# Optimization experiments

Hardware: AMD Instinct MI355X
Metric: run time of the kernel (lower is better)

Reference implementation:

```python
import jax, jax.numpy as jnp
import numpy as np

K_NBR = 64          # max_num_neighbors in radius()
RATIO1, R1 = 0.5, 0.2
RATIO2, R2 = 0.25, 0.4


def _mlp(h, params):
    # PyG MLP: Linear+ReLU per hidden layer, plain last layer (BN is identity at
    # init / eval with fresh running stats, so omitted).
    for w, b in params[:-1]:
        h = jax.nn.relu(h @ w + b)
    w, b = params[-1]
    return h @ w + b


def _fps(pos, S):
    # Farthest point sampling, deterministic start at index 0. pos: [N,3]
    min_d = jnp.sum((pos - pos[0]) ** 2, axis=-1)

    def body(md, _):
        i = jnp.argmax(md)
        md = jnp.minimum(md, jnp.sum((pos - pos[i]) ** 2, axis=-1))
        return md, i

    _, idxs = jax.lax.scan(body, min_d, None, length=S - 1)
    return jnp.concatenate([jnp.zeros((1,), idxs.dtype), idxs])  # [S]


def _sa(x, pos, S, r, params):
    # One SAModule for a single cloud. x: [N,C], pos: [N,3]
    sel = _fps(pos, S)
    pos_s = pos[sel]                                                   # [S,3]
    d2 = jnp.sum((pos_s[:, None, :] - pos[None, :, :]) ** 2, axis=-1)  # [S,N]
    score = jnp.where(d2 <= r * r, -d2, -jnp.inf)
    vals, nbr = jax.lax.top_k(score, K_NBR)      # <=64 nearest within radius r
    mask = vals > -jnp.inf                       # [S,K]; center always valid
    # PointNetConv message: cat([x_j, pos_j - pos_i]) -> local MLP -> max-aggr
    feats = jnp.concatenate([x[nbr], pos[nbr] - pos_s[:, None, :]], axis=-1)
    h = _mlp(feats, params)                      # [S,K,Cout]
    h = jnp.max(jnp.where(mask[..., None], h, -jnp.inf), axis=1)
    return h, pos_s


def _forward(data, p1, p2, p3, fc_w, fc_b):
    B, N, _ = data.shape
    S1 = int(np.ceil(N * RATIO1))
    S2 = int(np.ceil(S1 * RATIO2))
    # sa1 is called with x = pos = raw coordinates
    x1, pos1 = jax.vmap(lambda p: _sa(p, p, S1, R1, p1))(data)
    x2, pos2 = jax.vmap(lambda x, p: _sa(x, p, S2, R2, p2))(x1, pos1)
    # GlobalSAModule: MLP on cat([x, pos]) then global max pool per cloud
    g = jnp.max(_mlp(jnp.concatenate([x2, pos2], axis=-1), p3), axis=1)  # [B,1024]
    return g @ fc_w + fc_b


def setup_inputs() -> dict:
    key = jax.random.key(0)
    ks = jax.random.split(key, 16)
    B, N = 4, 4096
    inp = {"data": jax.random.uniform(ks[0], (B, N, 3), jnp.float32)}
    dims = {"sa1": [6, 64, 64, 128],
            "sa2": [131, 128, 128, 256],
            "sa3": [259, 256, 512, 1024]}
    i = 1
    for name, ds in dims.items():
        for l in range(len(ds) - 1):
            fi, fo = ds[l], ds[l + 1]
            inp[f"{name}_w{l + 1}"] = (jax.random.normal(ks[i], (fi, fo), jnp.float32)
                                       / np.float32(np.sqrt(fi)))
            inp[f"{name}_b{l + 1}"] = jnp.zeros((fo,), jnp.float32)
            i += 1
    inp["fc_w"] = jax.random.normal(ks[i], (1024, 256), jnp.float32) / np.float32(32.0)
    inp["fc_b"] = jnp.zeros((256,), jnp.float32)
    return inp


def reference(data, sa1_w1, sa1_b1, sa1_w2, sa1_b2, sa1_w3, sa1_b3,
              sa2_w1, sa2_b1, sa2_w2, sa2_b2, sa2_w3, sa2_b3,
              sa3_w1, sa3_b1, sa3_w2, sa3_b2, sa3_w3, sa3_b3,
              fc_w, fc_b):
    p1 = [(sa1_w1, sa1_b1), (sa1_w2, sa1_b2), (sa1_w3, sa1_b3)]
    p2 = [(sa2_w1, sa2_b1), (sa2_w2, sa2_b2), (sa2_w3, sa2_b3)]
    p3 = [(sa3_w1, sa3_b1), (sa3_w2, sa3_b2), (sa3_w3, sa3_b3)]
    return _forward(data, p1, p2, p3, fc_w, fc_b)  # [B, 256]
```

## Files before the change

kernel.cpp:

```cpp
#include <hip/hip_runtime.h>


#define DEVFN __device__ __forceinline__

DEVFN float d2_exact(float ax, float ay, float az, float bx, float by, float bz) {
    float dx = __fsub_rn(ax, bx);
    float dy = __fsub_rn(ay, by);
    float dz = __fsub_rn(az, bz);
    return __fadd_rn(__fadd_rn(__fmul_rn(dx, dx), __fmul_rn(dy, dy)), __fmul_rn(dz, dz));
}

DEVFN unsigned long long u64max(unsigned long long a, unsigned long long b) {
    return a > b ? a : b;
}

template <int R>
DEVFN unsigned long long dpp_ror16_u64(unsigned long long x) {
    int lo = (int)(unsigned)(x & 0xFFFFFFFFull);
    int hi = (int)(unsigned)(x >> 32);
    lo = __builtin_amdgcn_update_dpp(lo, lo, 0x120 | R, 0xF, 0xF, false);
    hi = __builtin_amdgcn_update_dpp(hi, hi, 0x120 | R, 0xF, 0xF, false);
    return ((unsigned long long)(unsigned)hi << 32) | (unsigned)lo;
}

DEVFN unsigned long long rl_u64(unsigned long long x, int lane) {
    unsigned l = (unsigned)__builtin_amdgcn_readlane((int)(unsigned)(x & 0xFFFFFFFFull), lane);
    unsigned h = (unsigned)__builtin_amdgcn_readlane((int)(unsigned)(x >> 32), lane);
    return ((unsigned long long)h << 32) | l;
}

template <int N, int S, int NT>
DEVFN void run_fps(const float* sx, const float* sy, const float* sz,
                   unsigned long long* sPack,
                   int* selLds) {
    constexpr int PPT = N / NT;
    constexpr int NW = NT / 64;
    const int tid = threadIdx.x;
    float px[PPT], py[PPT], pz[PPT], md[PPT];
    unsigned loc[PPT];
#pragma unroll
    for (int i = 0; i < PPT; ++i) {
        int idx = tid * PPT + i;
        px[i] = sx[idx]; py[i] = sy[idx]; pz[i] = sz[idx];
        md[i] = __builtin_inff();
        loc[i] = 0xFFFFFFFFu - (unsigned)idx;
    }
    if (tid == 0) selLds[0] = 0;
    int cur = 0;
    for (int s = 1; s < S; ++s) {
        float ax = sx[cur], ay = sy[cur], az = sz[cur];
        unsigned long long tq[PPT];
#pragma unroll
        for (int i = 0; i < PPT; ++i) {
            float d = d2_exact(px[i], py[i], pz[i], ax, ay, az);
            float m = fminf(md[i], d);
            md[i] = m;
            tq[i] = ((unsigned long long)__float_as_uint(m) << 32) |
                    (unsigned long long)loc[i];
        }
#pragma unroll
        for (int w = PPT / 2; w >= 1; w >>= 1)
#pragma unroll
            for (int i = 0; i < w; ++i) tq[i] = u64max(tq[i], tq[i + w]);

        unsigned long long pk = tq[0];
        pk = u64max(pk, dpp_ror16_u64<8>(pk));
        pk = u64max(pk, dpp_ror16_u64<4>(pk));
        pk = u64max(pk, dpp_ror16_u64<2>(pk));
        pk = u64max(pk, dpp_ror16_u64<1>(pk));

        unsigned long long wmax = u64max(u64max(rl_u64(pk, 0), rl_u64(pk, 16)),
                                         u64max(rl_u64(pk, 32), rl_u64(pk, 48)));

        unsigned long long* sp = sPack + (s & 1) * NW;
        if ((tid & 63) == 0) sp[tid >> 6] = wmax;
        __syncthreads();

        unsigned long long win;
        if constexpr (NW == 8) {
            const ulonglong2* sp2 = (const ulonglong2*)sp;
            ulonglong2 q0 = sp2[0], q1 = sp2[1], q2 = sp2[2], q3 = sp2[3];
            unsigned long long m01 = u64max(u64max(q0.x, q0.y), u64max(q1.x, q1.y));
            unsigned long long m23 = u64max(u64max(q2.x, q2.y), u64max(q3.x, q3.y));
            win = u64max(m01, m23);
        } else {
            const ulonglong2* sp2 = (const ulonglong2*)sp;
            ulonglong2 q0 = sp2[0], q1 = sp2[1];
            win = u64max(u64max(q0.x, q0.y), u64max(q1.x, q1.y));
        }

        cur = (int)(0xFFFFFFFFu - (unsigned)(win & 0xFFFFFFFFull));
        if (tid == 0) selLds[s] = cur;
    }
}

template <int N, int CAP>
DEVFN void nbr_body(const float* __restrict__ pos,
                    const float cx, const float cy, const float cz,
                    const float rsq, const int c,
                    int* __restrict__ nbr, int* __restrict__ cnt,
                    float* sDw, int* sIw) {
    const int lane = threadIdx.x & 63;
    int count = 0;
    for (int j = lane; j < N; j += 64) {
        float d = d2_exact(cx, cy, cz, pos[j * 3 + 0], pos[j * 3 + 1], pos[j * 3 + 2]);
        bool pred = (d <= rsq);
        unsigned long long m = __ballot(pred);
        int wpos = count + __popcll(m & ((1ull << lane) - 1ull));
        if (pred && wpos < CAP) { sDw[wpos] = d; sIw[wpos] = j; }
        count += __popcll(m);
    }
    if (count > CAP) count = CAP;

    for (int t = lane; t < count; t += 64) {
        float d = sDw[t]; int id = sIw[t];
        int rank = 0;
        int j0 = 0;
        for (; j0 + 4 <= count; j0 += 4) {
            float4 dj = *(const float4*)&sDw[j0];
            int4   ij = *(const int4*)&sIw[j0];
            rank += (dj.x < d || (dj.x == d && ij.x < id)) ? 1 : 0;
            rank += (dj.y < d || (dj.y == d && ij.y < id)) ? 1 : 0;
            rank += (dj.z < d || (dj.z == d && ij.z < id)) ? 1 : 0;
            rank += (dj.w < d || (dj.w == d && ij.w < id)) ? 1 : 0;
        }
        for (; j0 < count; ++j0) {
            float dj = sDw[j0]; int ij = sIw[j0];
            rank += (dj < d || (dj == d && ij < id)) ? 1 : 0;
        }
        if (rank < 64) nbr[(size_t)c * 64 + rank] = id;
    }
    if (lane == 0) cnt[c] = count < 64 ? count : 64;
}

__global__ __launch_bounds__(512) void fpsnbr_kernel(
    const float* __restrict__ data,
    float* __restrict__ mdG,
    int* __restrict__ selG,
    float* __restrict__ pos1,
    const int sb, const int se,
    const float rsq, int* __restrict__ nbr1, int* __restrict__ cnt1,
    const int s0)
{
    __shared__ __align__(16) char raw[65536];
    const int tid = threadIdx.x;

    if (blockIdx.x >= 4) {
        float* sD = (float*)raw;
        int*   sI = (int*)(raw + 32768);
        const int wid = tid >> 6;
        const int g = (int)(blockIdx.x - 4) * 8 + wid;
        const int b = g >> 9;
        const int s = s0 + (g & 511);
        const int c = b * 2048 + s;
        const float cx = pos1[(size_t)c * 3 + 0];
        const float cy = pos1[(size_t)c * 3 + 1];
        const float cz = pos1[(size_t)c * 3 + 2];
        nbr_body<4096, 1024>(data + (size_t)b * 4096 * 3, cx, cy, cz, rsq, c,
                             nbr1, cnt1, sD + wid * 1024, sI + wid * 1024);
        return;
    }

    constexpr int N = 4096, NT = 512, PPT = N / NT, NW = NT / 64;
    float* sx = (float*)raw;
    float* sy = sx + 4096;
    float* sz = sy + 4096;
    unsigned long long* sPack = (unsigned long long*)(raw + 49152);
    int* sSel = (int*)(raw + 49280);

    const int b = blockIdx.x;
    const float* p = data + (size_t)b * N * 3;
    for (int i = tid; i < N; i += NT) {
        sx[i] = p[i * 3 + 0]; sy[i] = p[i * 3 + 1]; sz[i] = p[i * 3 + 2];
    }
    __syncthreads();

    float px[PPT], py[PPT], pz[PPT], md[PPT];
    const bool first = (sb == 1);
#pragma unroll
    for (int i = 0; i < PPT; ++i) {
        int idx = tid * PPT + i;
        px[i] = sx[idx]; py[i] = sy[idx]; pz[i] = sz[idx];
        md[i] = first ? __builtin_inff() : mdG[(size_t)b * N + idx];
    }
    int cur = first ? 0 : selG[(size_t)b * 2048 + sb - 1];
    if (first && tid == 0) selG[(size_t)b * 2048] = 0;
    const unsigned lob = 0xFFFFFFFFu - (unsigned)(tid * PPT);

    for (int s = sb; s < se; ++s) {
        float ax = sx[cur], ay = sy[cur], az = sz[cur];
        float mm[PPT];
#pragma unroll
        for (int i = 0; i < PPT; ++i) {
            float d = d2_exact(px[i], py[i], pz[i], ax, ay, az);
            float m = fminf(md[i], d);
            md[i] = m; mm[i] = m;
        }
        float a0 = fmaxf(mm[0], mm[4]), a1 = fmaxf(mm[1], mm[5]);
        float a2 = fmaxf(mm[2], mm[6]), a3 = fmaxf(mm[3], mm[7]);
        float b0 = fmaxf(a0, a2), b1 = fmaxf(a1, a3);
        float mloc = fmaxf(b0, b1);
        int li = 7;
#pragma unroll
        for (int i = 6; i >= 0; --i) li = (mm[i] == mloc) ? i : li;

        unsigned long long k0 =
            ((unsigned long long)__float_as_uint(mloc) << 32) |
            (unsigned long long)(lob - (unsigned)li);

        k0 = u64max(k0, dpp_ror16_u64<8>(k0));
        k0 = u64max(k0, dpp_ror16_u64<4>(k0));
        k0 = u64max(k0, dpp_ror16_u64<2>(k0));
        k0 = u64max(k0, dpp_ror16_u64<1>(k0));

        unsigned long long wmax = u64max(u64max(rl_u64(k0, 0), rl_u64(k0, 16)),
                                         u64max(rl_u64(k0, 32), rl_u64(k0, 48)));

        unsigned long long* sp = sPack + (s & 1) * NW;
        if ((tid & 63) == 0) sp[tid >> 6] = wmax;
        __syncthreads();

        const ulonglong2* sp2 = (const ulonglong2*)sp;
        ulonglong2 q0 = sp2[0], q1 = sp2[1], q2 = sp2[2], q3 = sp2[3];
        unsigned long long m01 = u64max(u64max(q0.x, q0.y), u64max(q1.x, q1.y));
        unsigned long long m23 = u64max(u64max(q2.x, q2.y), u64max(q3.x, q3.y));
        unsigned long long win = u64max(m01, m23);

        cur = (int)(0xFFFFFFFFu - (unsigned)(win & 0xFFFFFFFFull));
        if (tid == 0) sSel[s - sb] = cur;
    }
    __syncthreads();

    if (se < 2048) {
#pragma unroll
        for (int i = 0; i < PPT; ++i)
            mdG[(size_t)b * N + tid * PPT + i] = md[i];
    }
    if (tid == 0) selG[(size_t)b * 2048 + se - 1] = cur;

    float* p1 = pos1 + (size_t)b * 2048 * 3;
    const int sb0 = first ? 0 : sb;
    for (int s = sb0 + tid; s < se; s += NT) {
        int idx = (s == 0) ? 0 : sSel[s - sb];
        p1[s * 3 + 0] = sx[idx]; p1[s * 3 + 1] = sy[idx]; p1[s * 3 + 2] = sz[idx];
    }
}

__global__ __launch_bounds__(512) void fps2nbr_kernel(
    const float* __restrict__ data,
    const float* __restrict__ pos1,
    float* __restrict__ pos2,
    const float rsq, int* __restrict__ nbr1, int* __restrict__ cnt1,
    const int s0)
{
    __shared__ __align__(16) char raw[65536];
    const int tid = threadIdx.x;

    if (blockIdx.x >= 4) {
        float* sD = (float*)raw;
        int*   sI = (int*)(raw + 32768);
        const int wid = tid >> 6;
        const int g = (int)(blockIdx.x - 4) * 8 + wid;
        const int b = g >> 9;
        const int s = s0 + (g & 511);
        const int c = b * 2048 + s;
        const float cx = pos1[(size_t)c * 3 + 0];
        const float cy = pos1[(size_t)c * 3 + 1];
        const float cz = pos1[(size_t)c * 3 + 2];
        nbr_body<4096, 1024>(data + (size_t)b * 4096 * 3, cx, cy, cz, rsq, c,
                             nbr1, cnt1, sD + wid * 1024, sI + wid * 1024);
        return;
    }

    float* sx = (float*)raw;
    float* sy = sx + 2048;
    float* sz = sy + 2048;
    int* sSel2 = (int*)(raw + 24576);
    unsigned long long* sPack2 = (unsigned long long*)(raw + 26624);

    const int b = blockIdx.x;
    const float* p1 = pos1 + (size_t)b * 2048 * 3;
    for (int i = tid; i < 2048; i += 512) {
        sx[i] = p1[i * 3 + 0]; sy[i] = p1[i * 3 + 1]; sz[i] = p1[i * 3 + 2];
    }
    __syncthreads();

    run_fps<2048, 512, 512>(sx, sy, sz, sPack2, sSel2);
    __syncthreads();

    float* p2 = pos2 + (size_t)b * 512 * 3;
    {
        int si = sSel2[tid];
        p2[tid * 3 + 0] = sx[si]; p2[tid * 3 + 1] = sy[si]; p2[tid * 3 + 2] = sz[si];
    }
}

DEVFN void tile44_fma(const float* __restrict__ aBase, int aStride,
                      const float* __restrict__ wBase, int wStride,
                      int nk4, float (&acc)[4][4]) {
    for (int k4 = 0; k4 < nk4; ++k4) {
        float a[4][4], w[4][4];
#pragma unroll
        for (int i = 0; i < 4; ++i) {
            float4 t = *(const float4*)(aBase + i * aStride + k4 * 4);
            a[i][0] = t.x; a[i][1] = t.y; a[i][2] = t.z; a[i][3] = t.w;
        }
#pragma unroll
        for (int kk = 0; kk < 4; ++kk) {
            float4 t = *(const float4*)(wBase + (size_t)(k4 * 4 + kk) * wStride);
            w[kk][0] = t.x; w[kk][1] = t.y; w[kk][2] = t.z; w[kk][3] = t.w;
        }
#pragma unroll
        for (int kk = 0; kk < 4; ++kk)
#pragma unroll
            for (int i = 0; i < 4; ++i)
#pragma unroll
                for (int j = 0; j < 4; ++j)
                    acc[i][j] = fmaf(a[i][kk], w[kk][j], acc[i][j]);
    }
}

DEVFN void tile48_fma(const float* __restrict__ aBase, int aStride,
                      const float* __restrict__ wBase, int wStride,
                      int nk4, float (&acc)[4][8]) {
    for (int k4 = 0; k4 < nk4; ++k4) {
        float a[4][4];
#pragma unroll
        for (int i = 0; i < 4; ++i) {
            float4 t = *(const float4*)(aBase + i * aStride + k4 * 4);
            a[i][0] = t.x; a[i][1] = t.y; a[i][2] = t.z; a[i][3] = t.w;
        }
#pragma unroll
        for (int kk = 0; kk < 4; ++kk) {
            float4 t0 = *(const float4*)(wBase + (size_t)(k4 * 4 + kk) * wStride);
            float4 t1 = *(const float4*)(wBase + (size_t)(k4 * 4 + kk) * wStride + 4);
            float w_[8] = {t0.x, t0.y, t0.z, t0.w, t1.x, t1.y, t1.z, t1.w};
#pragma unroll
            for (int i = 0; i < 4; ++i)
#pragma unroll
                for (int j = 0; j < 8; ++j)
                    acc[i][j] = fmaf(a[i][kk], w_[j], acc[i][j]);
        }
    }
}

__global__ __launch_bounds__(256) void mlp1nbr2_kernel(
    const float* __restrict__ pos,
    const float* __restrict__ ctr,
    const int* __restrict__ nbr, const int* __restrict__ cnt,
    const float* __restrict__ w1, const float* __restrict__ b1,
    const float* __restrict__ w2, const float* __restrict__ b2,
    const float* __restrict__ w3, const float* __restrict__ b3,
    float* __restrict__ x1,
    const float* __restrict__ pos1,
    const float* __restrict__ pos2,
    const float rsq2, int* __restrict__ nbr2, int* __restrict__ cnt2)
{
    __shared__ __align__(16) float smem[15424];
    const int tid = threadIdx.x;

    if (blockIdx.x < 512) {
        float* sD = smem;
        int*   sI = (int*)(smem + 6144);
        const int wid = tid >> 6;
        const int c = (int)blockIdx.x * 4 + wid;
        const int b = c >> 9;
        const float cx = pos2[(size_t)c * 3 + 0];
        const float cy = pos2[(size_t)c * 3 + 1];
        const float cz = pos2[(size_t)c * 3 + 2];
        nbr_body<2048, 1536>(pos1 + (size_t)b * 2048 * 3, cx, cy, cz, rsq2, c,
                             nbr2, cnt2, sD + wid * 1536, sI + wid * 1536);
        return;
    }

    float* sFeat = smem;
    float* sW    = smem + 576;
    float* sH1   = smem + 4672;
    float* sH2   = smem + 9024;
    float* sRed  = smem + 13376;

    const int c = blockIdx.x - 512;
    const int b = c >> 11;
    const int valid = cnt[c];

    if (tid < 64) {
        const int r = tid;
        float fx = 0.f, fy = 0.f, fz = 0.f, dx = 0.f, dy = 0.f, dz = 0.f;
        if (r < valid) {
            int j = nbr[(size_t)c * 64 + r];
            const float* pj = pos + ((size_t)b * 4096 + j) * 3;
            fx = pj[0]; fy = pj[1]; fz = pj[2];
            dx = fx - ctr[c * 3 + 0]; dy = fy - ctr[c * 3 + 1]; dz = fz - ctr[c * 3 + 2];
        }
        float* fr = sFeat + r * 9;
        fr[0] = fx; fr[1] = fy; fr[2] = fz; fr[3] = dx; fr[4] = dy; fr[5] = dz;
    }
    for (int l = tid; l < 4096; l += 256) sW[l] = w2[l];
    __syncthreads();

    {
        const int r = tid & 63, c0 = (tid >> 6) * 16;
        float acc[16];
#pragma unroll
        for (int q = 0; q < 16; ++q) acc[q] = b1[c0 + q];
#pragma unroll
        for (int k = 0; k < 6; ++k) {
            float a = sFeat[r * 9 + k];
#pragma unroll
            for (int q = 0; q < 16; ++q) acc[q] = fmaf(a, w1[k * 64 + c0 + q], acc[q]);
        }
        float* hr = sH1 + r * 68 + c0;
#pragma unroll
        for (int q = 0; q < 16; ++q) hr[q] = fmaxf(acc[q], 0.f);
    }
    __syncthreads();

    {
        const int r0 = (tid >> 4) * 4, c0 = (tid & 15) * 4;
        float acc[4][4];
#pragma unroll
        for (int i = 0; i < 4; ++i)
#pragma unroll
            for (int j = 0; j < 4; ++j) acc[i][j] = b2[c0 + j];
        tile44_fma(sH1 + r0 * 68, 68, sW + c0, 64, 16, acc);
#pragma unroll
        for (int i = 0; i < 4; ++i)
#pragma unroll
            for (int j = 0; j < 4; ++j)
                sH2[(r0 + i) * 68 + c0 + j] = fmaxf(acc[i][j], 0.f);
    }
    __syncthreads();

    for (int l = tid; l < 8192; l += 256) sW[l] = w3[l];
    __syncthreads();
    {
        const int r0 = (tid >> 4) * 4, c0 = (tid & 15) * 8;
        float acc[4][8];
#pragma unroll
        for (int i = 0; i < 4; ++i)
#pragma unroll
            for (int j = 0; j < 8; ++j) acc[i][j] = 0.f;
        tile48_fma(sH2 + r0 * 68, 68, sW + c0, 128, 16, acc);
        float pm[8];
#pragma unroll
        for (int j = 0; j < 8; ++j) pm[j] = -__builtin_inff();
#pragma unroll
        for (int i = 0; i < 4; ++i)
            if (r0 + i < valid)
#pragma unroll
                for (int j = 0; j < 8; ++j) pm[j] = fmaxf(pm[j], acc[i][j]);
#pragma unroll
        for (int j = 0; j < 8; ++j) sRed[(tid >> 4) * 128 + c0 + j] = pm[j];
    }
    __syncthreads();
    if (tid < 128) {
        float m = -__builtin_inff();
#pragma unroll
        for (int g = 0; g < 16; ++g) m = fmaxf(m, sRed[g * 128 + tid]);
        x1[(size_t)c * 128 + tid] = m + b3[tid];
    }
}

__global__ __launch_bounds__(512, 4) void mlp2_kernel(
    const float* __restrict__ x1,
    const float* __restrict__ pos1,
    const float* __restrict__ ctr,
    const int* __restrict__ nbr, const int* __restrict__ cnt,
    const float* __restrict__ w1, const float* __restrict__ b1,
    const float* __restrict__ w2, const float* __restrict__ b2,
    const float* __restrict__ w3, const float* __restrict__ b3,
    float* __restrict__ x2)
{
    __shared__ __align__(16) float sF[64 * 132];
    __shared__ __align__(16) float sH[64 * 132];
    float* sRed = sH;

    const int tid = threadIdx.x;
    const int c = blockIdx.x;
    const int b = c >> 9;
    const int valid = cnt[c];
    const float cx = ctr[c * 3 + 0], cy = ctr[c * 3 + 1], cz = ctr[c * 3 + 2];

    {
        const int r = tid >> 3, t8 = tid & 7;
        float* fr = sF + r * 132;
        if (r < valid) {
            int j = nbr[(size_t)c * 64 + r];
            const float* xp = x1 + ((size_t)b * 2048 + j) * 128;
#pragma unroll
            for (int q = 0; q < 4; ++q) {
                float4 v = *(const float4*)(xp + t8 * 16 + q * 4);
                fr[t8 * 16 + q * 4 + 0] = v.x; fr[t8 * 16 + q * 4 + 1] = v.y;
                fr[t8 * 16 + q * 4 + 2] = v.z; fr[t8 * 16 + q * 4 + 3] = v.w;
            }
            if (t8 == 0) {
                const float* pj = pos1 + ((size_t)b * 2048 + j) * 3;
                fr[128] = pj[0] - cx; fr[129] = pj[1] - cy; fr[130] = pj[2] - cz;
                fr[131] = 0.f;
            }
        } else {
#pragma unroll
            for (int q = 0; q < 16; ++q) fr[t8 * 16 + q] = 0.f;
            if (t8 == 0) { fr[128] = 0.f; fr[129] = 0.f; fr[130] = 0.f; fr[131] = 0.f; }
        }
    }
    __syncthreads();

    const int r0 = (tid >> 5) * 4;
    const int c0 = (tid & 31) * 4;
    const int c8 = (tid & 31) * 8;

    {
        float acc[4][4];
#pragma unroll
        for (int i = 0; i < 4; ++i)
#pragma unroll
            for (int j = 0; j < 4; ++j) acc[i][j] = b1[c0 + j];
        tile44_fma(sF + r0 * 132, 132, w1 + c0, 128, 32, acc);
        for (int k = 128; k < 131; ++k) {
            float4 wv = *(const float4*)(w1 + (size_t)k * 128 + c0);
            float w_[4] = {wv.x, wv.y, wv.z, wv.w};
#pragma unroll
            for (int i = 0; i < 4; ++i) {
                float a = sF[(r0 + i) * 132 + k];
#pragma unroll
                for (int j = 0; j < 4; ++j) acc[i][j] = fmaf(a, w_[j], acc[i][j]);
            }
        }
#pragma unroll
        for (int i = 0; i < 4; ++i)
#pragma unroll
            for (int j = 0; j < 4; ++j)
                sH[(r0 + i) * 132 + c0 + j] = fmaxf(acc[i][j], 0.f);
    }
    __syncthreads();

    {
        float acc[4][4];
#pragma unroll
        for (int i = 0; i < 4; ++i)
#pragma unroll
            for (int j = 0; j < 4; ++j) acc[i][j] = b2[c0 + j];
        tile44_fma(sH + r0 * 132, 132, w2 + c0, 128, 32, acc);
#pragma unroll
        for (int i = 0; i < 4; ++i)
#pragma unroll
            for (int j = 0; j < 4; ++j)
                sF[(r0 + i) * 132 + c0 + j] = fmaxf(acc[i][j], 0.f);
    }
    __syncthreads();

    {
        float acc[4][8];
#pragma unroll
        for (int i = 0; i < 4; ++i)
#pragma unroll
            for (int j = 0; j < 8; ++j) acc[i][j] = 0.f;
        tile48_fma(sF + r0 * 132, 132, w3 + c8, 256, 32, acc);
        float pm[8];
#pragma unroll
        for (int j = 0; j < 8; ++j) pm[j] = -__builtin_inff();
#pragma unroll
        for (int i = 0; i < 4; ++i)
            if (r0 + i < valid)
#pragma unroll
                for (int j = 0; j < 8; ++j) pm[j] = fmaxf(pm[j], acc[i][j]);
#pragma unroll
        for (int j = 0; j < 8; ++j) sRed[(tid >> 5) * 256 + c8 + j] = pm[j];
    }
    __syncthreads();
    if (tid < 256) {
        float m = -__builtin_inff();
#pragma unroll
        for (int g = 0; g < 16; ++g) m = fmaxf(m, sRed[g * 256 + tid]);
        x2[(size_t)c * 256 + tid] = m + b3[tid];
    }
}

__global__ __launch_bounds__(256) void gemm1f_kernel(const float* __restrict__ x2,
                                                     const float* __restrict__ pos2,
                                                     const float* __restrict__ W,
                                                     const float* __restrict__ bias,
                                                     float* __restrict__ C) {
    constexpr int K = 259, Nc = 256;
    __shared__ __align__(16) float sA[64 * 36];
    __shared__ __align__(16) float sB[32 * 68];
    const int tid = threadIdx.x;
    const int row0 = blockIdx.y * 64, col0 = blockIdx.x * 64;
    const int r0 = (tid >> 4) * 4, c0 = (tid & 15) * 4;
    float acc[4][4];
#pragma unroll
    for (int i = 0; i < 4; ++i)
#pragma unroll
        for (int j = 0; j < 4; ++j) acc[i][j] = 0.f;

    for (int kb = 0; kb < K; kb += 32) {
        for (int l = tid; l < 64 * 32; l += 256) {
            int r = l >> 5, k = l & 31;
            int gk = kb + k;
            float av = 0.f;
            if (gk < K) {
                int row = row0 + r;
                av = (gk < 256) ? x2[(size_t)row * 256 + gk]
                                : pos2[row * 3 + (gk - 256)];
            }
            sA[r * 36 + k] = av;
        }
        for (int l = tid; l < 32 * 64; l += 256) {
            int k = l >> 6, cc = l & 63;
            sB[k * 68 + cc] = (kb + k < K) ? W[(size_t)(kb + k) * Nc + col0 + cc] : 0.f;
        }
        __syncthreads();
        tile44_fma(sA + r0 * 36, 36, sB + c0, 68, 8, acc);
        __syncthreads();
    }
#pragma unroll
    for (int i = 0; i < 4; ++i)
#pragma unroll
        for (int j = 0; j < 4; ++j)
            C[(size_t)(row0 + r0 + i) * Nc + col0 + c0 + j] =
                fmaxf(acc[i][j] + bias[col0 + c0 + j], 0.f);
}

__global__ __launch_bounds__(256) void gemm_kernel(const float* __restrict__ A,
                                                   const float* __restrict__ W,
                                                   const float* __restrict__ bias,
                                                   float* __restrict__ C,
                                                   int M, int K, int Nc, int relu) {
    __shared__ __align__(16) float sA[64 * 36];
    __shared__ __align__(16) float sB[32 * 68];
    const int tid = threadIdx.x;
    const int row0 = blockIdx.y * 64, col0 = blockIdx.x * 64;
    const int r0 = (tid >> 4) * 4, c0 = (tid & 15) * 4;
    float acc[4][4];
#pragma unroll
    for (int i = 0; i < 4; ++i)
#pragma unroll
        for (int j = 0; j < 4; ++j) acc[i][j] = 0.f;

    for (int kb = 0; kb < K; kb += 32) {
        for (int l = tid; l < 64 * 32; l += 256) {
            int r = l >> 5, k = l & 31;
            sA[r * 36 + k] = (kb + k < K) ? A[(size_t)(row0 + r) * K + kb + k] : 0.f;
        }
        for (int l = tid; l < 32 * 64; l += 256) {
            int k = l >> 6, cc = l & 63;
            sB[k * 68 + cc] = (kb + k < K) ? W[(size_t)(kb + k) * Nc + col0 + cc] : 0.f;
        }
        __syncthreads();
        tile44_fma(sA + r0 * 36, 36, sB + c0, 68, 8, acc);
        __syncthreads();
    }
#pragma unroll
    for (int i = 0; i < 4; ++i)
#pragma unroll
        for (int j = 0; j < 4; ++j) {
            float v = acc[i][j] + bias[col0 + c0 + j];
            if (relu) v = fmaxf(v, 0.f);
            C[(size_t)(row0 + r0 + i) * Nc + col0 + c0 + j] = v;
        }
}

__global__ __launch_bounds__(1024) void mpfc_kernel(const float* __restrict__ h,
                                                    const float* __restrict__ w,
                                                    const float* __restrict__ bias,
                                                    float* __restrict__ out) {
    __shared__ float sG[1024];
    __shared__ float sP[4][256];
    const int b = blockIdx.x, tid = threadIdx.x;

    float m = -__builtin_inff();
    const float* hp = h + (size_t)b * 512 * 1024 + tid;
    for (int r = 0; r < 512; ++r) m = fmaxf(m, hp[(size_t)r * 1024]);
    sG[tid] = m;
    __syncthreads();

    const int c = tid & 255, kc = tid >> 8;
    float acc = 0.f;
    const float* wp = w + (size_t)(kc * 256) * 256 + c;
    const float* gp = sG + kc * 256;
    for (int k = 0; k < 256; ++k) acc = fmaf(gp[k], wp[(size_t)k * 256], acc);
    sP[kc][c] = acc;
    __syncthreads();
    if (tid < 256)
        out[b * 256 + tid] = ((sP[0][tid] + sP[1][tid]) + (sP[2][tid] + sP[3][tid]))
                             + bias[tid];
}

extern "C" void kernel_launch(void* const* d_in, const int* in_sizes, int n_in,
                              void* d_out, int out_size, void* d_ws, size_t ws_size,
                              hipStream_t stream) {
    const float* data  = (const float*)d_in[0];
    const float* s1w1  = (const float*)d_in[1];
    const float* s1b1  = (const float*)d_in[2];
    const float* s1w2  = (const float*)d_in[3];
    const float* s1b2  = (const float*)d_in[4];
    const float* s1w3  = (const float*)d_in[5];
    const float* s1b3  = (const float*)d_in[6];
    const float* s2w1  = (const float*)d_in[7];
    const float* s2b1  = (const float*)d_in[8];
    const float* s2w2  = (const float*)d_in[9];
    const float* s2b2  = (const float*)d_in[10];
    const float* s2w3  = (const float*)d_in[11];
    const float* s2b3  = (const float*)d_in[12];
    const float* s3w1  = (const float*)d_in[13];
    const float* s3b1  = (const float*)d_in[14];
    const float* s3w2  = (const float*)d_in[15];
    const float* s3b2  = (const float*)d_in[16];
    const float* s3w3  = (const float*)d_in[17];
    const float* s3b3  = (const float*)d_in[18];
    const float* fcw   = (const float*)d_in[19];
    const float* fcb   = (const float*)d_in[20];
    float* out = (float*)d_out;

    char* ws = (char*)d_ws;
    size_t o = 0;
    auto nxt = [&](size_t bytes) {
        size_t r = o;
        o += (bytes + 255) & ~(size_t)255;
        return r;
    };
    float* pos1 = (float*)(ws + nxt(4 * 2048 * 3 * 4));
    float* pos2 = (float*)(ws + nxt(4 * 512 * 3 * 4));
    float* mdG  = (float*)(ws + nxt(4 * 4096 * 4));
    int*   selG = (int*)(ws + nxt(4 * 2048 * 4));
    int*   nbr1 = (int*)(ws + nxt((size_t)8192 * 64 * 4));
    int*   cnt1 = (int*)(ws + nxt(8192 * 4));
    int*   nbr2 = (int*)(ws + nxt((size_t)2048 * 64 * 4));
    int*   cnt2 = (int*)(ws + nxt(2048 * 4));
    float* x1   = (float*)(ws + nxt((size_t)8192 * 128 * 4));
    float* x2   = (float*)(ws + nxt((size_t)2048 * 256 * 4));
    float* h1   = (float*)(ws + nxt((size_t)2048 * 256 * 4));
    float* h2   = (float*)(ws + nxt((size_t)2048 * 512 * 4));
    float* h3   = (float*)(ws + nxt((size_t)2048 * 1024 * 4));

    const float R1SQ = (float)(0.2 * 0.2);
    const float R2SQ = (float)(0.4 * 0.4);

    fpsnbr_kernel<<<4, 512, 0, stream>>>(data, mdG, selG, pos1, 1, 512,
                                         R1SQ, nbr1, cnt1, 0);
    fpsnbr_kernel<<<260, 512, 0, stream>>>(data, mdG, selG, pos1, 512, 1024,
                                           R1SQ, nbr1, cnt1, 0);
    fpsnbr_kernel<<<260, 512, 0, stream>>>(data, mdG, selG, pos1, 1024, 1536,
                                           R1SQ, nbr1, cnt1, 512);
    fpsnbr_kernel<<<260, 512, 0, stream>>>(data, mdG, selG, pos1, 1536, 2048,
                                           R1SQ, nbr1, cnt1, 1024);
    fps2nbr_kernel<<<260, 512, 0, stream>>>(data, pos1, pos2,
                                            R1SQ, nbr1, cnt1, 1536);
    mlp1nbr2_kernel<<<512 + 8192, 256, 0, stream>>>(data, pos1, nbr1, cnt1,
                                                    s1w1, s1b1, s1w2, s1b2,
                                                    s1w3, s1b3, x1,
                                                    pos1, pos2, R2SQ, nbr2, cnt2);
    mlp2_kernel<<<2048, 512, 0, stream>>>(x1, pos1, pos2, nbr2, cnt2,
                                          s2w1, s2b1, s2w2, s2b2, s2w3, s2b3, x2);
    gemm1f_kernel<<<dim3(4, 32), 256, 0, stream>>>(x2, pos2, s3w1, s3b1, h1);
    gemm_kernel<<<dim3(8, 32), 256, 0, stream>>>(h1, s3w2, s3b2, h2, 2048, 256, 512, 1);
    gemm_kernel<<<dim3(16, 32), 256, 0, stream>>>(h2, s3w3, s3b3, h3, 2048, 512, 1024, 0);
    mpfc_kernel<<<4, 1024, 0, stream>>>(h3, fcw, fcb, out);
}
```

Baseline: 2.647 ms.

## Overlap SA1 MLP chunks with serial FPS and neighbor search stages

Splits the SA1 MLP into per-chunk work and runs it in the same launches as the remaining FPS chunks and neighbor searches, so the MLP for already-grouped centers overlaps the serial 4-block FPS loop. The MLP body is also retiled for 512 threads, reading w2 and w3 directly from global memory instead of staging w2 in LDS. The stages are pipelined so each chunk's MLP runs one stage after its neighbors are found. Risks are more LDS per block (64 KB), lower occupancy for the MLP work, and interference with the latency-critical FPS blocks.

Result: slower. 4.255 ms (+60.7%).

```diff
diff --git a/kernel.cpp b/kernel.cpp
--- a/kernel.cpp
+++ b/kernel.cpp
@@ -29,10 +29,97 @@
     return ((unsigned long long)h << 32) | l;
 }
 
+DEVFN void fps_chunk_body(const float* __restrict__ data, float* __restrict__ mdG,
+                          int* __restrict__ selG, float* __restrict__ pos1,
+                          const int sb, const int se, char* raw) {
+    constexpr int N = 4096, NT = 512, PPT = N / NT, NW = NT / 64;
+    float* sx = (float*)raw;
+    float* sy = sx + 4096;
+    float* sz = sy + 4096;
+    unsigned long long* sPack = (unsigned long long*)(raw + 49152);
+    int* sSel = (int*)(raw + 49280);
+
+    const int b = blockIdx.x, tid = threadIdx.x;
+    const float* p = data + (size_t)b * N * 3;
+    for (int i = tid; i < N; i += NT) {
+        sx[i] = p[i * 3 + 0]; sy[i] = p[i * 3 + 1]; sz[i] = p[i * 3 + 2];
+    }
+    __syncthreads();
+
+    float px[PPT], py[PPT], pz[PPT], md[PPT];
+    const bool first = (sb == 1);
+#pragma unroll
+    for (int i = 0; i < PPT; ++i) {
+        int idx = tid * PPT + i;
+        px[i] = sx[idx]; py[i] = sy[idx]; pz[i] = sz[idx];
+        md[i] = first ? __builtin_inff() : mdG[(size_t)b * N + idx];
+    }
+    int cur = first ? 0 : selG[(size_t)b * 2048 + sb - 1];
+    if (first && tid == 0) selG[(size_t)b * 2048] = 0;
+    const unsigned lob = 0xFFFFFFFFu - (unsigned)(tid * PPT);
+
+    for (int s = sb; s < se; ++s) {
+        float ax = sx[cur], ay = sy[cur], az = sz[cur];
+        float mm[PPT];
+#pragma unroll
+        for (int i = 0; i < PPT; ++i) {
+            float d = d2_exact(px[i], py[i], pz[i], ax, ay, az);
+            float m = fminf(md[i], d);
+            md[i] = m; mm[i] = m;
+        }
+        float a0 = fmaxf(mm[0], mm[4]), a1 = fmaxf(mm[1], mm[5]);
+        float a2 = fmaxf(mm[2], mm[6]), a3 = fmaxf(mm[3], mm[7]);
+        float b0 = fmaxf(a0, a2), b1 = fmaxf(a1, a3);
+        float mloc = fmaxf(b0, b1);
+        int li = 7;
+#pragma unroll
+        for (int i = 6; i >= 0; --i) li = (mm[i] == mloc) ? i : li;
+
+        unsigned long long k0 =
+            ((unsigned long long)__float_as_uint(mloc) << 32) |
+            (unsigned long long)(lob - (unsigned)li);
+
+        k0 = u64max(k0, dpp_ror16_u64<8>(k0));
+        k0 = u64max(k0, dpp_ror16_u64<4>(k0));
+        k0 = u64max(k0, dpp_ror16_u64<2>(k0));
+        k0 = u64max(k0, dpp_ror16_u64<1>(k0));
+
+        unsigned long long wmax = u64max(u64max(rl_u64(k0, 0), rl_u64(k0, 16)),
+                                         u64max(rl_u64(k0, 32), rl_u64(k0, 48)));
+
+        unsigned long long* sp = sPack + (s & 1) * NW;
+        if ((tid & 63) == 0) sp[tid >> 6] = wmax;
+        __syncthreads();
+
+        const ulonglong2* sp2 = (const ulonglong2*)sp;
+        ulonglong2 q0 = sp2[0], q1 = sp2[1], q2 = sp2[2], q3 = sp2[3];
+        unsigned long long m01 = u64max(u64max(q0.x, q0.y), u64max(q1.x, q1.y));
+        unsigned long long m23 = u64max(u64max(q2.x, q2.y), u64max(q3.x, q3.y));
+        unsigned long long win = u64max(m01, m23);
+
+        cur = (int)(0xFFFFFFFFu - (unsigned)(win & 0xFFFFFFFFull));
+        if (tid == 0) sSel[s - sb] = cur;
+    }
+    __syncthreads();
+
+    if (se < 2048) {
+#pragma unroll
+        for (int i = 0; i < PPT; ++i)
+            mdG[(size_t)b * N + tid * PPT + i] = md[i];
+    }
+    if (tid == 0) selG[(size_t)b * 2048 + se - 1] = cur;
+
+    float* p1 = pos1 + (size_t)b * 2048 * 3;
+    const int sb0 = (sb == 1) ? 0 : sb;
+    for (int s = sb0 + tid; s < se; s += NT) {
+        int idx = (s == 0) ? 0 : sSel[s - sb];
+        p1[s * 3 + 0] = sx[idx]; p1[s * 3 + 1] = sy[idx]; p1[s * 3 + 2] = sz[idx];
+    }
+}
+
 template <int N, int S, int NT>
 DEVFN void run_fps(const float* sx, const float* sy, const float* sz,
-                   unsigned long long* sPack,
-                   int* selLds) {
+                   unsigned long long* sPack, int* selLds) {
     constexpr int PPT = N / NT;
     constexpr int NW = NT / 64;
     const int tid = threadIdx.x;
@@ -133,254 +220,17 @@
     if (lane == 0) cnt[c] = count < 64 ? count : 64;
 }
 
-__global__ __launch_bounds__(512) void fpsnbr_kernel(
-    const float* __restrict__ data,
-    float* __restrict__ mdG,
-    int* __restrict__ selG,
-    float* __restrict__ pos1,
-    const int sb, const int se,
-    const float rsq, int* __restrict__ nbr1, int* __restrict__ cnt1,
-    const int s0)
-{
-    __shared__ __align__(16) char raw[65536];
+DEVFN void mlp1_body(const float* __restrict__ pos, const float* __restrict__ ctr,
+                     const int* __restrict__ nbr, const int* __restrict__ cnt,
+                     const float* __restrict__ w1, const float* __restrict__ b1,
+                     const float* __restrict__ w2, const float* __restrict__ b2,
+                     const float* __restrict__ w3, const float* __restrict__ b3,
+                     float* __restrict__ x1, const int c, const int b, float* smemf) {
+    float* sFeat = smemf;
+    float* sH1   = smemf + 576;
+    float* sH2   = smemf + 4928;
+    float* sRed  = smemf + 9280;
     const int tid = threadIdx.x;
-
-    if (blockIdx.x >= 4) {
-        float* sD = (float*)raw;
-        int*   sI = (int*)(raw + 32768);
-        const int wid = tid >> 6;
-        const int g = (int)(blockIdx.x - 4) * 8 + wid;
-        const int b = g >> 9;
-        const int s = s0 + (g & 511);
-        const int c = b * 2048 + s;
-        const float cx = pos1[(size_t)c * 3 + 0];
-        const float cy = pos1[(size_t)c * 3 + 1];
-        const float cz = pos1[(size_t)c * 3 + 2];
-        nbr_body<4096, 1024>(data + (size_t)b * 4096 * 3, cx, cy, cz, rsq, c,
-                             nbr1, cnt1, sD + wid * 1024, sI + wid * 1024);
-        return;
-    }
-
-    constexpr int N = 4096, NT = 512, PPT = N / NT, NW = NT / 64;
-    float* sx = (float*)raw;
-    float* sy = sx + 4096;
-    float* sz = sy + 4096;
-    unsigned long long* sPack = (unsigned long long*)(raw + 49152);
-    int* sSel = (int*)(raw + 49280);
-
-    const int b = blockIdx.x;
-    const float* p = data + (size_t)b * N * 3;
-    for (int i = tid; i < N; i += NT) {
-        sx[i] = p[i * 3 + 0]; sy[i] = p[i * 3 + 1]; sz[i] = p[i * 3 + 2];
-    }
-    __syncthreads();
-
-    float px[PPT], py[PPT], pz[PPT], md[PPT];
-    const bool first = (sb == 1);
-#pragma unroll
-    for (int i = 0; i < PPT; ++i) {
-        int idx = tid * PPT + i;
-        px[i] = sx[idx]; py[i] = sy[idx]; pz[i] = sz[idx];
-        md[i] = first ? __builtin_inff() : mdG[(size_t)b * N + idx];
-    }
-    int cur = first ? 0 : selG[(size_t)b * 2048 + sb - 1];
-    if (first && tid == 0) selG[(size_t)b * 2048] = 0;
-    const unsigned lob = 0xFFFFFFFFu - (unsigned)(tid * PPT);
-
-    for (int s = sb; s < se; ++s) {
-        float ax = sx[cur], ay = sy[cur], az = sz[cur];
-        float mm[PPT];
-#pragma unroll
-        for (int i = 0; i < PPT; ++i) {
-            float d = d2_exact(px[i], py[i], pz[i], ax, ay, az);
-            float m = fminf(md[i], d);
-            md[i] = m; mm[i] = m;
-        }
-        float a0 = fmaxf(mm[0], mm[4]), a1 = fmaxf(mm[1], mm[5]);
-        float a2 = fmaxf(mm[2], mm[6]), a3 = fmaxf(mm[3], mm[7]);
-        float b0 = fmaxf(a0, a2), b1 = fmaxf(a1, a3);
-        float mloc = fmaxf(b0, b1);
-        int li = 7;
-#pragma unroll
-        for (int i = 6; i >= 0; --i) li = (mm[i] == mloc) ? i : li;
-
-        unsigned long long k0 =
-            ((unsigned long long)__float_as_uint(mloc) << 32) |
-            (unsigned long long)(lob - (unsigned)li);
-
-        k0 = u64max(k0, dpp_ror16_u64<8>(k0));
-        k0 = u64max(k0, dpp_ror16_u64<4>(k0));
-        k0 = u64max(k0, dpp_ror16_u64<2>(k0));
-        k0 = u64max(k0, dpp_ror16_u64<1>(k0));
-
-        unsigned long long wmax = u64max(u64max(rl_u64(k0, 0), rl_u64(k0, 16)),
-                                         u64max(rl_u64(k0, 32), rl_u64(k0, 48)));
-
-        unsigned long long* sp = sPack + (s & 1) * NW;
-        if ((tid & 63) == 0) sp[tid >> 6] = wmax;
-        __syncthreads();
-
-        const ulonglong2* sp2 = (const ulonglong2*)sp;
-        ulonglong2 q0 = sp2[0], q1 = sp2[1], q2 = sp2[2], q3 = sp2[3];
-        unsigned long long m01 = u64max(u64max(q0.x, q0.y), u64max(q1.x, q1.y));
-        unsigned long long m23 = u64max(u64max(q2.x, q2.y), u64max(q3.x, q3.y));
-        unsigned long long win = u64max(m01, m23);
-
-        cur = (int)(0xFFFFFFFFu - (unsigned)(win & 0xFFFFFFFFull));
-        if (tid == 0) sSel[s - sb] = cur;
-    }
-    __syncthreads();
-
-    if (se < 2048) {
-#pragma unroll
-        for (int i = 0; i < PPT; ++i)
-            mdG[(size_t)b * N + tid * PPT + i] = md[i];
-    }
-    if (tid == 0) selG[(size_t)b * 2048 + se - 1] = cur;
-
-    float* p1 = pos1 + (size_t)b * 2048 * 3;
-    const int sb0 = first ? 0 : sb;
-    for (int s = sb0 + tid; s < se; s += NT) {
-        int idx = (s == 0) ? 0 : sSel[s - sb];
-        p1[s * 3 + 0] = sx[idx]; p1[s * 3 + 1] = sy[idx]; p1[s * 3 + 2] = sz[idx];
-    }
-}
-
-__global__ __launch_bounds__(512) void fps2nbr_kernel(
-    const float* __restrict__ data,
-    const float* __restrict__ pos1,
-    float* __restrict__ pos2,
-    const float rsq, int* __restrict__ nbr1, int* __restrict__ cnt1,
-    const int s0)
-{
-    __shared__ __align__(16) char raw[65536];
-    const int tid = threadIdx.x;
-
-    if (blockIdx.x >= 4) {
-        float* sD = (float*)raw;
-        int*   sI = (int*)(raw + 32768);
-        const int wid = tid >> 6;
-        const int g = (int)(blockIdx.x - 4) * 8 + wid;
-        const int b = g >> 9;
-        const int s = s0 + (g & 511);
-        const int c = b * 2048 + s;
-        const float cx = pos1[(size_t)c * 3 + 0];
-        const float cy = pos1[(size_t)c * 3 + 1];
-        const float cz = pos1[(size_t)c * 3 + 2];
-        nbr_body<4096, 1024>(data + (size_t)b * 4096 * 3, cx, cy, cz, rsq, c,
-                             nbr1, cnt1, sD + wid * 1024, sI + wid * 1024);
-        return;
-    }
-
-    float* sx = (float*)raw;
-    float* sy = sx + 2048;
-    float* sz = sy + 2048;
-    int* sSel2 = (int*)(raw + 24576);
-    unsigned long long* sPack2 = (unsigned long long*)(raw + 26624);
-
-    const int b = blockIdx.x;
-    const float* p1 = pos1 + (size_t)b * 2048 * 3;
-    for (int i = tid; i < 2048; i += 512) {
-        sx[i] = p1[i * 3 + 0]; sy[i] = p1[i * 3 + 1]; sz[i] = p1[i * 3 + 2];
-    }
-    __syncthreads();
-
-    run_fps<2048, 512, 512>(sx, sy, sz, sPack2, sSel2);
-    __syncthreads();
-
-    float* p2 = pos2 + (size_t)b * 512 * 3;
-    {
-        int si = sSel2[tid];
-        p2[tid * 3 + 0] = sx[si]; p2[tid * 3 + 1] = sy[si]; p2[tid * 3 + 2] = sz[si];
-    }
-}
-
-DEVFN void tile44_fma(const float* __restrict__ aBase, int aStride,
-                      const float* __restrict__ wBase, int wStride,
-                      int nk4, float (&acc)[4][4]) {
-    for (int k4 = 0; k4 < nk4; ++k4) {
-        float a[4][4], w[4][4];
-#pragma unroll
-        for (int i = 0; i < 4; ++i) {
-            float4 t = *(const float4*)(aBase + i * aStride + k4 * 4);
-            a[i][0] = t.x; a[i][1] = t.y; a[i][2] = t.z; a[i][3] = t.w;
-        }
-#pragma unroll
-        for (int kk = 0; kk < 4; ++kk) {
-            float4 t = *(const float4*)(wBase + (size_t)(k4 * 4 + kk) * wStride);
-            w[kk][0] = t.x; w[kk][1] = t.y; w[kk][2] = t.z; w[kk][3] = t.w;
-        }
-#pragma unroll
-        for (int kk = 0; kk < 4; ++kk)
-#pragma unroll
-            for (int i = 0; i < 4; ++i)
-#pragma unroll
-                for (int j = 0; j < 4; ++j)
-                    acc[i][j] = fmaf(a[i][kk], w[kk][j], acc[i][j]);
-    }
-}
-
-DEVFN void tile48_fma(const float* __restrict__ aBase, int aStride,
-                      const float* __restrict__ wBase, int wStride,
-                      int nk4, float (&acc)[4][8]) {
-    for (int k4 = 0; k4 < nk4; ++k4) {
-        float a[4][4];
-#pragma unroll
-        for (int i = 0; i < 4; ++i) {
-            float4 t = *(const float4*)(aBase + i * aStride + k4 * 4);
-            a[i][0] = t.x; a[i][1] = t.y; a[i][2] = t.z; a[i][3] = t.w;
-        }
-#pragma unroll
-        for (int kk = 0; kk < 4; ++kk) {
-            float4 t0 = *(const float4*)(wBase + (size_t)(k4 * 4 + kk) * wStride);
-            float4 t1 = *(const float4*)(wBase + (size_t)(k4 * 4 + kk) * wStride + 4);
-            float w_[8] = {t0.x, t0.y, t0.z, t0.w, t1.x, t1.y, t1.z, t1.w};
-#pragma unroll
-            for (int i = 0; i < 4; ++i)
-#pragma unroll
-                for (int j = 0; j < 8; ++j)
-                    acc[i][j] = fmaf(a[i][kk], w_[j], acc[i][j]);
-        }
-    }
-}
-
-__global__ __launch_bounds__(256) void mlp1nbr2_kernel(
-    const float* __restrict__ pos,
-    const float* __restrict__ ctr,
-    const int* __restrict__ nbr, const int* __restrict__ cnt,
-    const float* __restrict__ w1, const float* __restrict__ b1,
-    const float* __restrict__ w2, const float* __restrict__ b2,
-    const float* __restrict__ w3, const float* __restrict__ b3,
-    float* __restrict__ x1,
-    const float* __restrict__ pos1,
-    const float* __restrict__ pos2,
-    const float rsq2, int* __restrict__ nbr2, int* __restrict__ cnt2)
-{
-    __shared__ __align__(16) float smem[15424];
-    const int tid = threadIdx.x;
-
-    if (blockIdx.x < 512) {
-        float* sD = smem;
-        int*   sI = (int*)(smem + 6144);
-        const int wid = tid >> 6;
-        const int c = (int)blockIdx.x * 4 + wid;
-        const int b = c >> 9;
-        const float cx = pos2[(size_t)c * 3 + 0];
-        const float cy = pos2[(size_t)c * 3 + 1];
-        const float cz = pos2[(size_t)c * 3 + 2];
-        nbr_body<2048, 1536>(pos1 + (size_t)b * 2048 * 3, cx, cy, cz, rsq2, c,
-                             nbr2, cnt2, sD + wid * 1536, sI + wid * 1536);
-        return;
-    }
-
-    float* sFeat = smem;
-    float* sW    = smem + 576;
-    float* sH1   = smem + 4672;
-    float* sH2   = smem + 9024;
-    float* sRed  = smem + 13376;
-
-    const int c = blockIdx.x - 512;
-    const int b = c >> 11;
     const int valid = cnt[c];
 
     if (tid < 64) {
@@ -395,62 +245,89 @@
         float* fr = sFeat + r * 9;
         fr[0] = fx; fr[1] = fy; fr[2] = fz; fr[3] = dx; fr[4] = dy; fr[5] = dz;
     }
-    for (int l = tid; l < 4096; l += 256) sW[l] = w2[l];
     __syncthreads();
 
     {
-        const int r = tid & 63, c0 = (tid >> 6) * 16;
-        float acc[16];
-#pragma unroll
-        for (int q = 0; q < 16; ++q) acc[q] = b1[c0 + q];
+        const int r = tid & 63, c0 = (tid >> 6) * 8;
+        float acc[8];
+#pragma unroll
+        for (int q = 0; q < 8; ++q) acc[q] = b1[c0 + q];
 #pragma unroll
         for (int k = 0; k < 6; ++k) {
             float a = sFeat[r * 9 + k];
 #pragma unroll
-            for (int q = 0; q < 16; ++q) acc[q] = fmaf(a, w1[k * 64 + c0 + q], acc[q]);
+            for (int q = 0; q < 8; ++q) acc[q] = fmaf(a, w1[k * 64 + c0 + q], acc[q]);
         }
         float* hr = sH1 + r * 68 + c0;
 #pragma unroll
-        for (int q = 0; q < 16; ++q) hr[q] = fmaxf(acc[q], 0.f);
+        for (int q = 0; q < 8; ++q) hr[q] = fmaxf(acc[q], 0.f);
     }
     __syncthreads();
 
     {
-        const int r0 = (tid >> 4) * 4, c0 = (tid & 15) * 4;
+        const int rg = tid >> 4, c0 = (tid & 15) * 4;
+        float acc0[4], acc1[4];
+#pragma unroll
+        for (int j = 0; j < 4; ++j) { acc0[j] = b2[c0 + j]; acc1[j] = b2[c0 + j]; }
+        for (int k4 = 0; k4 < 16; ++k4) {
+            float4 t0 = *(const float4*)(sH1 + rg * 68 + k4 * 4);
+            float4 t1 = *(const float4*)(sH1 + (rg + 32) * 68 + k4 * 4);
+            float a0_[4] = {t0.x, t0.y, t0.z, t0.w};
+            float a1_[4] = {t1.x, t1.y, t1.z, t1.w};
+#pragma unroll
+            for (int kk = 0; kk < 4; ++kk) {
+                float4 wv = *(const float4*)(w2 + (size_t)(k4 * 4 + kk) * 64 + c0);
+                float w_[4] = {wv.x, wv.y, wv.z, wv.w};
+#pragma unroll
+                for (int j = 0; j < 4; ++j) {
+                    acc0[j] = fmaf(a0_[kk], w_[j], acc0[j]);
+                    acc1[j] = fmaf(a1_[kk], w_[j], acc1[j]);
+                }
+            }
+        }
+#pragma unroll
+        for (int j = 0; j < 4; ++j) {
+            sH2[rg * 68 + c0 + j]        = fmaxf(acc0[j], 0.f);
+            sH2[(rg + 32) * 68 + c0 + j] = fmaxf(acc1[j], 0.f);
+        }
+    }
+    __syncthreads();
+
+    {
+        const int rg = tid >> 5, c0 = (tid & 31) * 4;
         float acc[4][4];
 #pragma unroll
         for (int i = 0; i < 4; ++i)
 #pragma unroll
-            for (int j = 0; j < 4; ++j) acc[i][j] = b2[c0 + j];
-        tile44_fma(sH1 + r0 * 68, 68, sW + c0, 64, 16, acc);
+            for (int j = 0; j < 4; ++j) acc[i][j] = 0.f;
+        for (int k4 = 0; k4 < 16; ++k4) {
+            float a[4][4];
+#pragma unroll
+            for (int i = 0; i < 4; ++i) {
+                float4 t = *(const float4*)(sH2 + (rg + 16 * i) * 68 + k4 * 4);
+                a[i][0] = t.x; a[i][1] = t.y; a[i][2] = t.z; a[i][3] = t.w;
+            }
+#pragma unroll
+            for (int kk = 0; kk < 4; ++kk) {
+                float4 wv = *(const float4*)(w3 + (size_t)(k4 * 4 + kk) * 128 + c0);
+                float w_[4] = {wv.x, wv.y, wv.z, wv.w};
+#pragma unroll
+                for (int i = 0; i < 4; ++i)
+#pragma unroll
+                    for (int j = 0; j < 4; ++j)
+                        acc[i][j] = fmaf(a[i][kk], w_[j], acc[i][j]);
+            }
+        }
+        float pm[4];
+#pragma unroll
+        for (int j = 0; j < 4; ++j) pm[j] = -__builtin_inff();
 #pragma unroll
         for (int i = 0; i < 4; ++i)
-#pragma unroll
-            for (int j = 0; j < 4; ++j)
-                sH2[(r0 + i) * 68 + c0 + j] = fmaxf(acc[i][j], 0.f);
-    }
-    __syncthreads();
-
-    for (int l = tid; l < 8192; l += 256) sW[l] = w3[l];
-    __syncthreads();
-    {
-        const int r0 = (tid >> 4) * 4, c0 = (tid & 15) * 8;
-        float acc[4][8];
-#pragma unroll
-        for (int i = 0; i < 4; ++i)
-#pragma unroll
-            for (int j = 0; j < 8; ++j) acc[i][j] = 0.f;
-        tile48_fma(sH2 + r0 * 68, 68, sW + c0, 128, 16, acc);
-        float pm[8];
-#pragma unroll
-        for (int j = 0; j < 8; ++j) pm[j] = -__builtin_inff();
-#pragma unroll
-        for (int i = 0; i < 4; ++i)
-            if (r0 + i < valid)
-#pragma unroll
-                for (int j = 0; j < 8; ++j) pm[j] = fmaxf(pm[j], acc[i][j]);
-#pragma unroll
-        for (int j = 0; j < 8; ++j) sRed[(tid >> 4) * 128 + c0 + j] = pm[j];
+            if (rg + 16 * i < valid)
+#pragma unroll
+                for (int j = 0; j < 4; ++j) pm[j] = fmaxf(pm[j], acc[i][j]);
+#pragma unroll
+        for (int j = 0; j < 4; ++j) sRed[rg * 128 + c0 + j] = pm[j];
     }
     __syncthreads();
     if (tid < 128) {
@@ -461,9 +338,173 @@
     }
 }
 
+__global__ __launch_bounds__(512) void stageA_kernel(
+    const float* __restrict__ data, float* __restrict__ mdG,
+    int* __restrict__ selG, float* __restrict__ pos1,
+    const int sb, const int se,
+    const float rsq, int* __restrict__ nbr1, int* __restrict__ cnt1, const int s0n,
+    const float* __restrict__ w1, const float* __restrict__ b1,
+    const float* __restrict__ w2, const float* __restrict__ b2,
+    const float* __restrict__ w3, const float* __restrict__ b3,
+    float* __restrict__ x1, const int s0m)
+{
+    __shared__ __align__(16) char raw[65536];
+    if (blockIdx.x < 4) {
+        fps_chunk_body(data, mdG, selG, pos1, sb, se, raw);
+        return;
+    }
+    if (blockIdx.x < 260) {
+        float* sD = (float*)raw;
+        int*   sI = (int*)(raw + 32768);
+        const int wid = threadIdx.x >> 6;
+        const int g = (int)(blockIdx.x - 4) * 8 + wid;
+        const int b = g >> 9;
+        const int s = s0n + (g & 511);
+        const int c = b * 2048 + s;
+        nbr_body<4096, 1024>(data + (size_t)b * 4096 * 3,
+                             pos1[(size_t)c * 3 + 0], pos1[(size_t)c * 3 + 1],
+                             pos1[(size_t)c * 3 + 2], rsq, c,
+                             nbr1, cnt1, sD + wid * 1024, sI + wid * 1024);
+        return;
+    }
+    const int g = (int)blockIdx.x - 260;
+    const int b = g >> 9;
+    const int c = b * 2048 + s0m + (g & 511);
+    mlp1_body(data, pos1, nbr1, cnt1, w1, b1, w2, b2, w3, b3, x1, c, b, (float*)raw);
+}
+
+__global__ __launch_bounds__(512) void stageB_kernel(
+    const float* __restrict__ data, const float* __restrict__ pos1,
+    float* __restrict__ pos2,
+    const float rsq, int* __restrict__ nbr1, int* __restrict__ cnt1, const int s0n,
+    const float* __restrict__ w1, const float* __restrict__ b1,
+    const float* __restrict__ w2, const float* __restrict__ b2,
+    const float* __restrict__ w3, const float* __restrict__ b3,
+    float* __restrict__ x1, const int s0m)
+{
+    __shared__ __align__(16) char raw[65536];
+    const int tid = threadIdx.x;
+    if (blockIdx.x < 4) {
+        float* sx = (float*)raw;
+        float* sy = sx + 2048;
+        float* sz = sy + 2048;
+        int* sSel2 = (int*)(raw + 24576);
+        unsigned long long* sPack2 = (unsigned long long*)(raw + 26624);
+        const int b = blockIdx.x;
+        const float* p1 = pos1 + (size_t)b * 2048 * 3;
+        for (int i = tid; i < 2048; i += 512) {
+            sx[i] = p1[i * 3 + 0]; sy[i] = p1[i * 3 + 1]; sz[i] = p1[i * 3 + 2];
+        }
+        __syncthreads();
+        run_fps<2048, 512, 512>(sx, sy, sz, sPack2, sSel2);
+        __syncthreads();
+        float* p2 = pos2 + (size_t)b * 512 * 3;
+        int si = sSel2[tid];
+        p2[tid * 3 + 0] = sx[si]; p2[tid * 3 + 1] = sy[si]; p2[tid * 3 + 2] = sz[si];
+        return;
+    }
+    if (blockIdx.x < 260) {
+        float* sD = (float*)raw;
+        int*   sI = (int*)(raw + 32768);
+        const int wid = tid >> 6;
+        const int g = (int)(blockIdx.x - 4) * 8 + wid;
+        const int b = g >> 9;
+        const int s = s0n + (g & 511);
+        const int c = b * 2048 + s;
+        nbr_body<4096, 1024>(data + (size_t)b * 4096 * 3,
+                             pos1[(size_t)c * 3 + 0], pos1[(size_t)c * 3 + 1],
+                             pos1[(size_t)c * 3 + 2], rsq, c,
+                             nbr1, cnt1, sD + wid * 1024, sI + wid * 1024);
+        return;
+    }
+    const int g = (int)blockIdx.x - 260;
+    const int b = g >> 9;
+    const int c = b * 2048 + s0m + (g & 511);
+    mlp1_body(data, pos1, nbr1, cnt1, w1, b1, w2, b2, w3, b3, x1, c, b, (float*)raw);
+}
+
+__global__ __launch_bounds__(512) void stageC_kernel(
+    const float* __restrict__ data, const float* __restrict__ pos1,
+    const float* __restrict__ pos2,
+    const float rsq2, int* __restrict__ nbr2, int* __restrict__ cnt2,
+    const int* __restrict__ nbr1, const int* __restrict__ cnt1,
+    const float* __restrict__ w1, const float* __restrict__ b1,
+    const float* __restrict__ w2, const float* __restrict__ b2,
+    const float* __restrict__ w3, const float* __restrict__ b3,
+    float* __restrict__ x1, const int s0m)
+{
+    __shared__ __align__(16) char raw[65536];
+    const int tid = threadIdx.x;
+    if (blockIdx.x < 512) {
+        const int wid = tid >> 6;
+        if (wid >= 4) return;
+        float* sD = (float*)raw;
+        int*   sI = (int*)(raw + 24576);
+        const int c = (int)blockIdx.x * 4 + wid;
+        const int b = c >> 9;
+        nbr_body<2048, 1536>(pos1 + (size_t)b * 2048 * 3,
+                             pos2[(size_t)c * 3 + 0], pos2[(size_t)c * 3 + 1],
+                             pos2[(size_t)c * 3 + 2], rsq2, c,
+                             nbr2, cnt2, sD + wid * 1536, sI + wid * 1536);
+        return;
+    }
+    const int g = (int)blockIdx.x - 512;
+    const int b = g >> 9;
+    const int c = b * 2048 + s0m + (g & 511);
+    mlp1_body(data, pos1, nbr1, cnt1, w1, b1, w2, b2, w3, b3, x1, c, b, (float*)raw);
+}
+
+DEVFN void tile44_fma(const float* __restrict__ aBase, int aStride,
+                      const float* __restrict__ wBase, int wStride,
+                      int nk4, float (&acc)[4][4]) {
+    for (int k4 = 0; k4 < nk4; ++k4) {
+        float a[4][4], w[4][4];
+#pragma unroll
+        for (int i = 0; i < 4; ++i) {
+            float4 t = *(const float4*)(aBase + i * aStride + k4 * 4);
+            a[i][0] = t.x; a[i][1] = t.y; a[i][2] = t.z; a[i][3] = t.w;
+        }
+#pragma unroll
+        for (int kk = 0; kk < 4; ++kk) {
+            float4 t = *(const float4*)(wBase + (size_t)(k4 * 4 + kk) * wStride);
+            w[kk][0] = t.x; w[kk][1] = t.y; w[kk][2] = t.z; w[kk][3] = t.w;
+        }
+#pragma unroll
+        for (int kk = 0; kk < 4; ++kk)
+#pragma unroll
+            for (int i = 0; i < 4; ++i)
+#pragma unroll
+                for (int j = 0; j < 4; ++j)
+                    acc[i][j] = fmaf(a[i][kk], w[kk][j], acc[i][j]);
+    }
+}
+
+DEVFN void tile48_fma(const float* __restrict__ aBase, int aStride,
+                      const float* __restrict__ wBase, int wStride,
+                      int nk4, float (&acc)[4][8]) {
+    for (int k4 = 0; k4 < nk4; ++k4) {
+        float a[4][4];
+#pragma unroll
+        for (int i = 0; i < 4; ++i) {
+            float4 t = *(const float4*)(aBase + i * aStride + k4 * 4);
+            a[i][0] = t.x; a[i][1] = t.y; a[i][2] = t.z; a[i][3] = t.w;
+        }
+#pragma unroll
+        for (int kk = 0; kk < 4; ++kk) {
+            float4 t0 = *(const float4*)(wBase + (size_t)(k4 * 4 + kk) * wStride);
+            float4 t1 = *(const float4*)(wBase + (size_t)(k4 * 4 + kk) * wStride + 4);
+            float w_[8] = {t0.x, t0.y, t0.z, t0.w, t1.x, t1.y, t1.z, t1.w};
+#pragma unroll
+            for (int i = 0; i < 4; ++i)
+#pragma unroll
+                for (int j = 0; j < 8; ++j)
+                    acc[i][j] = fmaf(a[i][kk], w_[j], acc[i][j]);
+        }
+    }
+}
+
 __global__ __launch_bounds__(512, 4) void mlp2_kernel(
-    const float* __restrict__ x1,
-    const float* __restrict__ pos1,
+    const float* __restrict__ x1, const float* __restrict__ pos1,
     const float* __restrict__ ctr,
     const int* __restrict__ nbr, const int* __restrict__ cnt,
     const float* __restrict__ w1, const float* __restrict__ b1,
@@ -737,20 +778,24 @@
     const float R1SQ = (float)(0.2 * 0.2);
     const float R2SQ = (float)(0.4 * 0.4);
 
-    fpsnbr_kernel<<<4, 512, 0, stream>>>(data, mdG, selG, pos1, 1, 512,
-                                         R1SQ, nbr1, cnt1, 0);
-    fpsnbr_kernel<<<260, 512, 0, stream>>>(data, mdG, selG, pos1, 512, 1024,
-                                           R1SQ, nbr1, cnt1, 0);
-    fpsnbr_kernel<<<260, 512, 0, stream>>>(data, mdG, selG, pos1, 1024, 1536,
-                                           R1SQ, nbr1, cnt1, 512);
-    fpsnbr_kernel<<<260, 512, 0, stream>>>(data, mdG, selG, pos1, 1536, 2048,
-                                           R1SQ, nbr1, cnt1, 1024);
-    fps2nbr_kernel<<<260, 512, 0, stream>>>(data, pos1, pos2,
-                                            R1SQ, nbr1, cnt1, 1536);
-    mlp1nbr2_kernel<<<512 + 8192, 256, 0, stream>>>(data, pos1, nbr1, cnt1,
-                                                    s1w1, s1b1, s1w2, s1b2,
-                                                    s1w3, s1b3, x1,
-                                                    pos1, pos2, R2SQ, nbr2, cnt2);
+    stageA_kernel<<<4, 512, 0, stream>>>(data, mdG, selG, pos1, 1, 512,
+                                         R1SQ, nbr1, cnt1, 0,
+                                         s1w1, s1b1, s1w2, s1b2, s1w3, s1b3, x1, 0);
+    stageA_kernel<<<260, 512, 0, stream>>>(data, mdG, selG, pos1, 512, 1024,
+                                           R1SQ, nbr1, cnt1, 0,
+                                           s1w1, s1b1, s1w2, s1b2, s1w3, s1b3, x1, 0);
+    stageA_kernel<<<2308, 512, 0, stream>>>(data, mdG, selG, pos1, 1024, 1536,
+                                            R1SQ, nbr1, cnt1, 512,
+                                            s1w1, s1b1, s1w2, s1b2, s1w3, s1b3, x1, 0);
+    stageA_kernel<<<2308, 512, 0, stream>>>(data, mdG, selG, pos1, 1536, 2048,
+                                            R1SQ, nbr1, cnt1, 1024,
+                                            s1w1, s1b1, s1w2, s1b2, s1w3, s1b3, x1, 512);
+    stageB_kernel<<<2308, 512, 0, stream>>>(data, pos1, pos2,
+                                            R1SQ, nbr1, cnt1, 1536,
+                                            s1w1, s1b1, s1w2, s1b2, s1w3, s1b3, x1, 1024);
+    stageC_kernel<<<2560, 512, 0, stream>>>(data, pos1, pos2,
+                                            R2SQ, nbr2, cnt2, nbr1, cnt1,
+                                            s1w1, s1b1, s1w2, s1b2, s1w3, s1b3, x1, 1536);
     mlp2_kernel<<<2048, 512, 0, stream>>>(x1, pos1, pos2, nbr2, cnt2,
                                           s2w1, s2b1, s2w2, s2b2, s2w3, s2b3, x2);
     gemm1f_kernel<<<dim3(4, 32), 256, 0, stream>>>(x2, pos2, s3w1, s3b1, h1);
```
